# Optimization experiments

Hardware: AMD Instinct MI355X
Metric: run time of the kernel (lower is better)

The kernel has to match this reference:

```python
import jax, jax.numpy as jnp
import numpy as np

B = 131072      # batch size
H = 300         # hidden_dim (per-source), se has 2*H = 600 columns
T = 2           # num_source_tasks
EPS = 1e-20


def setup_inputs() -> dict:
    key = jax.random.key(0)
    k1, k2, k3, k4, k5 = jax.random.split(key, 5)
    return {
        "se1": jax.random.normal(k1, (B, H), dtype=jnp.float32),
        "se2": jax.random.normal(k2, (B, H), dtype=jnp.float32),
        "W": jax.random.normal(k3, (T, 2 * H), dtype=jnp.float32) / np.sqrt(2 * H).astype(np.float32),
        "b": jax.random.normal(k4, (T,), dtype=jnp.float32),
        "u": jax.random.uniform(k5, (B, T), dtype=jnp.float32),
        "n_tasks": 2,
    }


def reference(se1, se2, W, b, u, n_tasks):
    # se = torch.cat(se, dim=1) -> [B, 2H]
    se = jnp.concatenate([se1, se2], axis=1)
    # tiny linear + relu + log_softmax
    se_postrelu = jax.nn.relu(se @ W.T + b)            # [B, T]
    logits = jax.nn.log_softmax(se_postrelu, axis=1)   # [B, T]
    # straight-through gumbel-softmax (temperature=1.0, no mask)
    gumbel = -jnp.log(-jnp.log(u + EPS) + EPS)
    y = jax.nn.softmax(logits + gumbel, axis=1)        # soft probs
    y_hard = jax.nn.one_hot(jnp.argmax(y, axis=1), T, dtype=y.dtype)
    selector = jax.lax.stop_gradient(y_hard - y) + y   # ST estimator, [B, T]
    # rf: first H cols = selector[:,0], next H cols = selector[:,1]
    rf = jnp.repeat(selector, H, axis=1)               # [B, 2H]
    return se * rf
```

## Files before the change

### kernel.cpp

```cpp
#include <hip/hip_runtime.h>
#include <math.h>

#define BDIM 256
#define WPB (BDIM / 64)

__global__ __launch_bounds__(BDIM) void taskselector_kernel(
    const float* __restrict__ se1,
    const float* __restrict__ se2,
    const float* __restrict__ W,
    const float* __restrict__ bvec,
    const float* __restrict__ u,
    float* __restrict__ out,
    int Brows)
{
    const int lane   = threadIdx.x & 63;
    const int waveid = threadIdx.x >> 6;
    const int wglob  = blockIdx.x * WPB + waveid;
    const int nwaves = gridDim.x * WPB;

    const float4 zero4 = make_float4(0.f, 0.f, 0.f, 0.f);
    const bool extra = (lane < 11);

    const float4* W0 = reinterpret_cast<const float4*>(W);
    const float4* W1 = reinterpret_cast<const float4*>(W + 600);
    float4 w0a = W0[lane];
    float4 w0b = extra ? W0[64 + lane]  : zero4;
    float4 w0c = W0[75 + lane];
    float4 w0d = extra ? W0[139 + lane] : zero4;
    float4 w1a = W1[lane];
    float4 w1b = extra ? W1[64 + lane]  : zero4;
    float4 w1c = W1[75 + lane];
    float4 w1d = extra ? W1[139 + lane] : zero4;
    const float b0 = bvec[0];
    const float b1 = bvec[1];

    for (int row = wglob; row < Brows; row += nwaves) {
        const float4* p1 = reinterpret_cast<const float4*>(se1 + (size_t)row * 300);
        const float4* p2 = reinterpret_cast<const float4*>(se2 + (size_t)row * 300);

        float4 a0 = p1[lane];
        float4 a1 = extra ? p1[64 + lane] : zero4;
        float4 c0 = p2[lane];
        float4 c1 = extra ? p2[64 + lane] : zero4;

        float d0 = a0.x * w0a.x + a0.y * w0a.y + a0.z * w0a.z + a0.w * w0a.w
                 + a1.x * w0b.x + a1.y * w0b.y + a1.z * w0b.z + a1.w * w0b.w
                 + c0.x * w0c.x + c0.y * w0c.y + c0.z * w0c.z + c0.w * w0c.w
                 + c1.x * w0d.x + c1.y * w0d.y + c1.z * w0d.z + c1.w * w0d.w;
        float d1 = a0.x * w1a.x + a0.y * w1a.y + a0.z * w1a.z + a0.w * w1a.w
                 + a1.x * w1b.x + a1.y * w1b.y + a1.z * w1b.z + a1.w * w1b.w
                 + c0.x * w1c.x + c0.y * w1c.y + c0.z * w1c.z + c0.w * w1c.w
                 + c1.x * w1d.x + c1.y * w1d.y + c1.z * w1d.z + c1.w * w1d.w;

        #pragma unroll
        for (int off = 32; off > 0; off >>= 1) {
            d0 += __shfl_xor(d0, off, 64);
            d1 += __shfl_xor(d1, off, 64);
        }

        float z0 = fmaxf(d0 + b0, 0.f);
        float z1 = fmaxf(d1 + b1, 0.f);

        float m   = fmaxf(z0, z1);
        float lse = m + logf(expf(z0 - m) + expf(z1 - m));
        float l0  = z0 - lse;
        float l1  = z1 - lse;

        float u0 = u[(size_t)row * 2 + 0];
        float u1 = u[(size_t)row * 2 + 1];
        float g0 = -logf(-logf(u0 + 1e-20f) + 1e-20f);
        float g1 = -logf(-logf(u1 + 1e-20f) + 1e-20f);

        float q0 = l0 + g0;
        float q1 = l1 + g1;
        float mm = fmaxf(q0, q1);
        float e0 = expf(q0 - mm);
        float e1 = expf(q1 - mm);
        float s  = e0 + e1;
        float y0 = e0 / s;
        float y1 = e1 / s;

        bool  pick0 = (q0 >= q1);
        float s0 = pick0 ? ((1.f - y0) + y0) : 0.f;
        float s1 = pick0 ? 0.f : ((1.f - y1) + y1);

        float4* o = reinterpret_cast<float4*>(out + (size_t)row * 600);
        float4 r;
        r.x = a0.x * s0; r.y = a0.y * s0; r.z = a0.z * s0; r.w = a0.w * s0;
        o[lane] = r;
        if (extra) {
            r.x = a1.x * s0; r.y = a1.y * s0; r.z = a1.z * s0; r.w = a1.w * s0;
            o[64 + lane] = r;
        }
        r.x = c0.x * s1; r.y = c0.y * s1; r.z = c0.z * s1; r.w = c0.w * s1;
        o[75 + lane] = r;
        if (extra) {
            r.x = c1.x * s1; r.y = c1.y * s1; r.z = c1.z * s1; r.w = c1.w * s1;
            o[139 + lane] = r;
        }
    }
}

extern "C" void kernel_launch(void* const* d_in, const int* in_sizes, int n_in,
                              void* d_out, int out_size, void* d_ws, size_t ws_size,
                              hipStream_t stream) {
    const float* se1 = (const float*)d_in[0];
    const float* se2 = (const float*)d_in[1];
    const float* W   = (const float*)d_in[2];
    const float* b   = (const float*)d_in[3];
    const float* u   = (const float*)d_in[4];
    float* out = (float*)d_out;

    const int Brows = in_sizes[0] / 300;

    int blocks = 2048;
    int maxBlocks = (Brows + WPB - 1) / WPB;
    if (blocks > maxBlocks) blocks = maxBlocks;

    taskselector_kernel<<<blocks, BDIM, 0, stream>>>(se1, se2, W, b, u, out, Brows);
}
```

Baseline: 132.3 us.

## Process row pairs per wave with software-pipelined loads and nontemporal memory ops

Each wave now handles two rows at a time and works through a contiguous block of pairs instead of a strided set of rows. The next pair's loads are issued before the current pair is computed, giving a double-buffered software pipeline. Loads and stores use nontemporal hints, and the grid shrinks from 2048 to 512 blocks. The aim is more memory requests in flight per wave on a bandwidth-bound streaming kernel, at the cost of higher register pressure and fewer resident waves.

```diff
diff --git a/kernel.cpp b/kernel.cpp
--- a/kernel.cpp
+++ b/kernel.cpp
@@ -1,8 +1,103 @@
 #include <hip/hip_runtime.h>
 #include <math.h>
 
+typedef float f4 __attribute__((ext_vector_type(4)));
+
 #define BDIM 256
 #define WPB (BDIM / 64)
+#define NBLOCKS 512
+
+struct Pair {
+    f4 aA0, aA1, cA0, cA1, aB0, aB1, cB0, cB1, uu;
+};
+
+struct WReg {
+    f4 w0a, w0b, w0c, w0d, w1a, w1b, w1c, w1d;
+    float b0, b1;
+};
+
+__device__ __forceinline__ float dot4(f4 a, f4 w) {
+    return a[0]*w[0] + a[1]*w[1] + a[2]*w[2] + a[3]*w[3];
+}
+
+__device__ __forceinline__ void load_pair(Pair& P,
+        const float* __restrict__ se1, const float* __restrict__ se2,
+        const float* __restrict__ u, int pairIdx, int lane, bool extra)
+{
+    const int rowA = pairIdx * 2;
+    const f4* pA1 = (const f4*)(se1 + (size_t)rowA * 300);
+    const f4* pA2 = (const f4*)(se2 + (size_t)rowA * 300);
+    const f4* pB1 = pA1 + 75;
+    const f4* pB2 = pA2 + 75;
+    const f4 zero = (f4)0.f;
+    P.aA0 = __builtin_nontemporal_load(pA1 + lane);
+    P.cA0 = __builtin_nontemporal_load(pA2 + lane);
+    P.aB0 = __builtin_nontemporal_load(pB1 + lane);
+    P.cB0 = __builtin_nontemporal_load(pB2 + lane);
+    P.aA1 = zero; P.cA1 = zero; P.aB1 = zero; P.cB1 = zero;
+    if (extra) {
+        P.aA1 = __builtin_nontemporal_load(pA1 + 64 + lane);
+        P.cA1 = __builtin_nontemporal_load(pA2 + 64 + lane);
+        P.aB1 = __builtin_nontemporal_load(pB1 + 64 + lane);
+        P.cB1 = __builtin_nontemporal_load(pB2 + 64 + lane);
+    }
+    P.uu = *(const f4*)(u + (size_t)rowA * 2);
+}
+
+__device__ __forceinline__ void epilogue_row(float d0, float d1, float u0, float u1,
+                                             float b0, float b1, float& s0, float& s1)
+{
+    float z0 = fmaxf(d0 + b0, 0.f);
+    float z1 = fmaxf(d1 + b1, 0.f);
+    float m  = fmaxf(z0, z1);
+    float lse = m + logf(expf(z0 - m) + expf(z1 - m));
+    float q0 = (z0 - lse) + (-logf(-logf(u0 + 1e-20f) + 1e-20f));
+    float q1 = (z1 - lse) + (-logf(-logf(u1 + 1e-20f) + 1e-20f));
+    float mm = fmaxf(q0, q1);
+    float e0 = expf(q0 - mm);
+    float e1 = expf(q1 - mm);
+    float s  = e0 + e1;
+    float y0 = e0 / s;
+    float y1 = e1 / s;
+    bool  pick0 = (q0 >= q1);
+    s0 = pick0 ? ((1.f - y0) + y0) : 0.f;
+    s1 = pick0 ? 0.f : ((1.f - y1) + y1);
+}
+
+__device__ __forceinline__ void proc_pair(const Pair& P, const WReg& WR,
+        float* __restrict__ out, int pairIdx, int lane, bool extra)
+{
+    float dA0 = dot4(P.aA0, WR.w0a) + dot4(P.aA1, WR.w0b) + dot4(P.cA0, WR.w0c) + dot4(P.cA1, WR.w0d);
+    float dA1 = dot4(P.aA0, WR.w1a) + dot4(P.aA1, WR.w1b) + dot4(P.cA0, WR.w1c) + dot4(P.cA1, WR.w1d);
+    float dB0 = dot4(P.aB0, WR.w0a) + dot4(P.aB1, WR.w0b) + dot4(P.cB0, WR.w0c) + dot4(P.cB1, WR.w0d);
+    float dB1 = dot4(P.aB0, WR.w1a) + dot4(P.aB1, WR.w1b) + dot4(P.cB0, WR.w1c) + dot4(P.cB1, WR.w1d);
+
+    #pragma unroll
+    for (int off = 32; off > 0; off >>= 1) {
+        dA0 += __shfl_xor(dA0, off, 64);
+        dA1 += __shfl_xor(dA1, off, 64);
+        dB0 += __shfl_xor(dB0, off, 64);
+        dB1 += __shfl_xor(dB1, off, 64);
+    }
+
+    float sA0, sA1, sB0, sB1;
+    epilogue_row(dA0, dA1, P.uu[0], P.uu[1], WR.b0, WR.b1, sA0, sA1);
+    epilogue_row(dB0, dB1, P.uu[2], P.uu[3], WR.b0, WR.b1, sB0, sB1);
+
+    const int rowA = pairIdx * 2;
+    f4* oA = (f4*)(out + (size_t)rowA * 600);
+    f4* oB = oA + 150;
+    __builtin_nontemporal_store(P.aA0 * sA0, oA + lane);
+    __builtin_nontemporal_store(P.cA0 * sA1, oA + 75 + lane);
+    __builtin_nontemporal_store(P.aB0 * sB0, oB + lane);
+    __builtin_nontemporal_store(P.cB0 * sB1, oB + 75 + lane);
+    if (extra) {
+        __builtin_nontemporal_store(P.aA1 * sA0, oA + 64 + lane);
+        __builtin_nontemporal_store(P.cA1 * sA1, oA + 139 + lane);
+        __builtin_nontemporal_store(P.aB1 * sB0, oB + 64 + lane);
+        __builtin_nontemporal_store(P.cB1 * sB1, oB + 139 + lane);
+    }
+}
 
 __global__ __launch_bounds__(BDIM) void taskselector_kernel(
     const float* __restrict__ se1,
@@ -16,87 +111,73 @@
     const int lane   = threadIdx.x & 63;
     const int waveid = threadIdx.x >> 6;
     const int wglob  = blockIdx.x * WPB + waveid;
-    const int nwaves = gridDim.x * WPB;
-
-    const float4 zero4 = make_float4(0.f, 0.f, 0.f, 0.f);
+    const int nw     = gridDim.x * WPB;
     const bool extra = (lane < 11);
-
-    const float4* W0 = reinterpret_cast<const float4*>(W);
-    const float4* W1 = reinterpret_cast<const float4*>(W + 600);
-    float4 w0a = W0[lane];
-    float4 w0b = extra ? W0[64 + lane]  : zero4;
-    float4 w0c = W0[75 + lane];
-    float4 w0d = extra ? W0[139 + lane] : zero4;
-    float4 w1a = W1[lane];
-    float4 w1b = extra ? W1[64 + lane]  : zero4;
-    float4 w1c = W1[75 + lane];
-    float4 w1d = extra ? W1[139 + lane] : zero4;
-    const float b0 = bvec[0];
-    const float b1 = bvec[1];
-
-    for (int row = wglob; row < Brows; row += nwaves) {
-        const float4* p1 = reinterpret_cast<const float4*>(se1 + (size_t)row * 300);
-        const float4* p2 = reinterpret_cast<const float4*>(se2 + (size_t)row * 300);
-
-        float4 a0 = p1[lane];
-        float4 a1 = extra ? p1[64 + lane] : zero4;
-        float4 c0 = p2[lane];
-        float4 c1 = extra ? p2[64 + lane] : zero4;
-
-        float d0 = a0.x * w0a.x + a0.y * w0a.y + a0.z * w0a.z + a0.w * w0a.w
-                 + a1.x * w0b.x + a1.y * w0b.y + a1.z * w0b.z + a1.w * w0b.w
-                 + c0.x * w0c.x + c0.y * w0c.y + c0.z * w0c.z + c0.w * w0c.w
-                 + c1.x * w0d.x + c1.y * w0d.y + c1.z * w0d.z + c1.w * w0d.w;
-        float d1 = a0.x * w1a.x + a0.y * w1a.y + a0.z * w1a.z + a0.w * w1a.w
-                 + a1.x * w1b.x + a1.y * w1b.y + a1.z * w1b.z + a1.w * w1b.w
-                 + c0.x * w1c.x + c0.y * w1c.y + c0.z * w1c.z + c0.w * w1c.w
-                 + c1.x * w1d.x + c1.y * w1d.y + c1.z * w1d.z + c1.w * w1d.w;
-
+    const f4 zero = (f4)0.f;
+
+    WReg WR;
+    const f4* W0 = (const f4*)(W);
+    const f4* W1 = (const f4*)(W + 600);
+    WR.w0a = W0[lane];
+    WR.w0b = extra ? W0[64 + lane]  : zero;
+    WR.w0c = W0[75 + lane];
+    WR.w0d = extra ? W0[139 + lane] : zero;
+    WR.w1a = W1[lane];
+    WR.w1b = extra ? W1[64 + lane]  : zero;
+    WR.w1c = W1[75 + lane];
+    WR.w1d = extra ? W1[139 + lane] : zero;
+    WR.b0 = bvec[0];
+    WR.b1 = bvec[1];
+
+    const int pairsTotal = Brows >> 1;
+    const int ppw = pairsTotal / nw;
+    const int rem = pairsTotal - ppw * nw;
+    int i   = wglob * ppw + (wglob < rem ? wglob : rem);
+    int cnt = ppw + (wglob < rem ? 1 : 0);
+
+    if (cnt > 0) {
+        const int end = i + cnt;
+        Pair X, Y;
+        load_pair(X, se1, se2, u, i, lane, extra);
+        while (i + 2 < end) {
+            load_pair(Y, se1, se2, u, i + 1, lane, extra);
+            proc_pair(X, WR, out, i, lane, extra);
+            load_pair(X, se1, se2, u, i + 2, lane, extra);
+            proc_pair(Y, WR, out, i + 1, lane, extra);
+            i += 2;
+        }
+        if (end - i == 2) {
+            load_pair(Y, se1, se2, u, i + 1, lane, extra);
+            proc_pair(X, WR, out, i, lane, extra);
+            proc_pair(Y, WR, out, i + 1, lane, extra);
+        } else {
+            proc_pair(X, WR, out, i, lane, extra);
+        }
+    }
+
+    if ((Brows & 1) && wglob == 0) {
+        const int row = Brows - 1;
+        const f4* p1 = (const f4*)(se1 + (size_t)row * 300);
+        const f4* p2 = (const f4*)(se2 + (size_t)row * 300);
+        f4 a0 = p1[lane];
+        f4 c0 = p2[lane];
+        f4 a1 = extra ? p1[64 + lane] : zero;
+        f4 c1 = extra ? p2[64 + lane] : zero;
+        float d0 = dot4(a0, WR.w0a) + dot4(a1, WR.w0b) + dot4(c0, WR.w0c) + dot4(c1, WR.w0d);
+        float d1 = dot4(a0, WR.w1a) + dot4(a1, WR.w1b) + dot4(c0, WR.w1c) + dot4(c1, WR.w1d);
         #pragma unroll
         for (int off = 32; off > 0; off >>= 1) {
             d0 += __shfl_xor(d0, off, 64);
             d1 += __shfl_xor(d1, off, 64);
         }
-
-        float z0 = fmaxf(d0 + b0, 0.f);
-        float z1 = fmaxf(d1 + b1, 0.f);
-
-        float m   = fmaxf(z0, z1);
-        float lse = m + logf(expf(z0 - m) + expf(z1 - m));
-        float l0  = z0 - lse;
-        float l1  = z1 - lse;
-
-        float u0 = u[(size_t)row * 2 + 0];
-        float u1 = u[(size_t)row * 2 + 1];
-        float g0 = -logf(-logf(u0 + 1e-20f) + 1e-20f);
-        float g1 = -logf(-logf(u1 + 1e-20f) + 1e-20f);
-
-        float q0 = l0 + g0;
-        float q1 = l1 + g1;
-        float mm = fmaxf(q0, q1);
-        float e0 = expf(q0 - mm);
-        float e1 = expf(q1 - mm);
-        float s  = e0 + e1;
-        float y0 = e0 / s;
-        float y1 = e1 / s;
-
-        bool  pick0 = (q0 >= q1);
-        float s0 = pick0 ? ((1.f - y0) + y0) : 0.f;
-        float s1 = pick0 ? 0.f : ((1.f - y1) + y1);
-
-        float4* o = reinterpret_cast<float4*>(out + (size_t)row * 600);
-        float4 r;
-        r.x = a0.x * s0; r.y = a0.y * s0; r.z = a0.z * s0; r.w = a0.w * s0;
-        o[lane] = r;
+        float s0, s1;
+        epilogue_row(d0, d1, u[(size_t)row * 2], u[(size_t)row * 2 + 1], WR.b0, WR.b1, s0, s1);
+        f4* o = (f4*)(out + (size_t)row * 600);
+        o[lane] = a0 * s0;
+        o[75 + lane] = c0 * s1;
         if (extra) {
-            r.x = a1.x * s0; r.y = a1.y * s0; r.z = a1.z * s0; r.w = a1.w * s0;
-            o[64 + lane] = r;
-        }
-        r.x = c0.x * s1; r.y = c0.y * s1; r.z = c0.z * s1; r.w = c0.w * s1;
-        o[75 + lane] = r;
-        if (extra) {
-            r.x = c1.x * s1; r.y = c1.y * s1; r.z = c1.z * s1; r.w = c1.w * s1;
-            o[139 + lane] = r;
+            o[64 + lane]  = a1 * s0;
+            o[139 + lane] = c1 * s1;
         }
     }
 }
@@ -113,8 +194,8 @@
 
     const int Brows = in_sizes[0] / 300;
 
-    int blocks = 2048;
-    int maxBlocks = (Brows + WPB - 1) / WPB;
+    int blocks = NBLOCKS;
+    int maxBlocks = ((Brows >> 1) + WPB - 1) / WPB;
     if (blocks > maxBlocks) blocks = maxBlocks;
 
     taskselector_kernel<<<blocks, BDIM, 0, stream>>>(se1, se2, W, b, u, out, Brows);
```

After: 142.5 us. +7.7%, slower.

## Stage 16-row tiles in LDS with coalesced nontemporal loads and stores

Applied to the files above, without the earlier changes.

Each block now takes a 16-row tile and loads it with fully coalesced nontemporal float4 loads into shared memory. Dot products and the selector are computed from LDS, and the output is written back as one contiguous coalesced nontemporal stream, with one block per tile instead of a grid-stride loop over rows. This removes partially idle lanes and scattered 1200-byte row accesses, and bypasses cache for streaming data. In exchange it uses about 38KB of LDS per block, which limits occupancy, adds two barriers, and assumes the batch size is divisible by 16.

```diff
diff --git a/kernel.cpp b/kernel.cpp
--- a/kernel.cpp
+++ b/kernel.cpp
@@ -1,121 +1,146 @@
 #include <hip/hip_runtime.h>
 #include <math.h>
 
+typedef float f4 __attribute__((ext_vector_type(4)));
+
 #define BDIM 256
-#define WPB (BDIM / 64)
+#define TROWS 16
+#define RPW 4
+#define TILE_F4_IN 1200
+#define TILE_F4_OUT 2400
+
+__device__ __forceinline__ float dot4(f4 a, f4 w) {
+    return a[0]*w[0] + a[1]*w[1] + a[2]*w[2] + a[3]*w[3];
+}
 
 __global__ __launch_bounds__(BDIM) void taskselector_kernel(
-    const float* __restrict__ se1,
-    const float* __restrict__ se2,
+    const f4* __restrict__ se1,
+    const f4* __restrict__ se2,
     const float* __restrict__ W,
     const float* __restrict__ bvec,
-    const float* __restrict__ u,
-    float* __restrict__ out,
-    int Brows)
+    const f4* __restrict__ u4,
+    f4* __restrict__ out)
 {
-    const int lane   = threadIdx.x & 63;
-    const int waveid = threadIdx.x >> 6;
-    const int wglob  = blockIdx.x * WPB + waveid;
-    const int nwaves = gridDim.x * WPB;
+    __shared__ f4 L1[TILE_F4_IN];
+    __shared__ f4 L2[TILE_F4_IN];
+    __shared__ float SEL[TROWS * 2];
+    __shared__ f4 UL[TROWS / 2];
 
-    const float4 zero4 = make_float4(0.f, 0.f, 0.f, 0.f);
+    const int tid  = threadIdx.x;
+    const int lane = tid & 63;
+    const int wave = tid >> 6;
+    const int tile = blockIdx.x;
+
     const bool extra = (lane < 11);
-
-    const float4* W0 = reinterpret_cast<const float4*>(W);
-    const float4* W1 = reinterpret_cast<const float4*>(W + 600);
-    float4 w0a = W0[lane];
-    float4 w0b = extra ? W0[64 + lane]  : zero4;
-    float4 w0c = W0[75 + lane];
-    float4 w0d = extra ? W0[139 + lane] : zero4;
-    float4 w1a = W1[lane];
-    float4 w1b = extra ? W1[64 + lane]  : zero4;
-    float4 w1c = W1[75 + lane];
-    float4 w1d = extra ? W1[139 + lane] : zero4;
+    const f4 zero = (f4)0.f;
+    const f4* W0 = (const f4*)W;
+    const f4* W1 = (const f4*)(W + 600);
+    f4 w0a = W0[lane];
+    f4 w0b = extra ? W0[64 + lane]  : zero;
+    f4 w0c = W0[75 + lane];
+    f4 w0d = extra ? W0[139 + lane] : zero;
+    f4 w1a = W1[lane];
+    f4 w1b = extra ? W1[64 + lane]  : zero;
+    f4 w1c = W1[75 + lane];
+    f4 w1d = extra ? W1[139 + lane] : zero;
     const float b0 = bvec[0];
     const float b1 = bvec[1];
 
-    for (int row = wglob; row < Brows; row += nwaves) {
-        const float4* p1 = reinterpret_cast<const float4*>(se1 + (size_t)row * 300);
-        const float4* p2 = reinterpret_cast<const float4*>(se2 + (size_t)row * 300);
+    const f4* s1 = se1 + (size_t)tile * TILE_F4_IN;
+    const f4* s2 = se2 + (size_t)tile * TILE_F4_IN;
+    f4 t[4], q[4];
+    #pragma unroll
+    for (int k = 0; k < 4; k++) t[k] = __builtin_nontemporal_load(s1 + k * BDIM + tid);
+    #pragma unroll
+    for (int k = 0; k < 4; k++) q[k] = __builtin_nontemporal_load(s2 + k * BDIM + tid);
+    f4 t4 = zero, q4 = zero;
+    if (tid < TILE_F4_IN - 4 * BDIM) {
+        t4 = __builtin_nontemporal_load(s1 + 4 * BDIM + tid);
+        q4 = __builtin_nontemporal_load(s2 + 4 * BDIM + tid);
+    }
+    if (tid < TROWS / 2) UL[tid] = u4[(size_t)tile * (TROWS / 2) + tid];
+    #pragma unroll
+    for (int k = 0; k < 4; k++) L1[k * BDIM + tid] = t[k];
+    #pragma unroll
+    for (int k = 0; k < 4; k++) L2[k * BDIM + tid] = q[k];
+    if (tid < TILE_F4_IN - 4 * BDIM) {
+        L1[4 * BDIM + tid] = t4;
+        L2[4 * BDIM + tid] = q4;
+    }
+    __syncthreads();
 
-        float4 a0 = p1[lane];
-        float4 a1 = extra ? p1[64 + lane] : zero4;
-        float4 c0 = p2[lane];
-        float4 c1 = extra ? p2[64 + lane] : zero4;
-
-        float d0 = a0.x * w0a.x + a0.y * w0a.y + a0.z * w0a.z + a0.w * w0a.w
-                 + a1.x * w0b.x + a1.y * w0b.y + a1.z * w0b.z + a1.w * w0b.w
-                 + c0.x * w0c.x + c0.y * w0c.y + c0.z * w0c.z + c0.w * w0c.w
-                 + c1.x * w0d.x + c1.y * w0d.y + c1.z * w0d.z + c1.w * w0d.w;
-        float d1 = a0.x * w1a.x + a0.y * w1a.y + a0.z * w1a.z + a0.w * w1a.w
-                 + a1.x * w1b.x + a1.y * w1b.y + a1.z * w1b.z + a1.w * w1b.w
-                 + c0.x * w1c.x + c0.y * w1c.y + c0.z * w1c.z + c0.w * w1c.w
-                 + c1.x * w1d.x + c1.y * w1d.y + c1.z * w1d.z + c1.w * w1d.w;
-
+    const float* ULf = (const float*)UL;
+    #pragma unroll
+    for (int rr = 0; rr < RPW; rr++) {
+        const int r = wave * RPW + rr;
+        const f4* R1 = L1 + r * 75;
+        const f4* R2 = L2 + r * 75;
+        f4 a0 = R1[lane];
+        f4 c0 = R2[lane];
+        f4 a1 = extra ? R1[64 + lane] : zero;
+        f4 c1 = extra ? R2[64 + lane] : zero;
+        float d0 = dot4(a0, w0a) + dot4(a1, w0b) + dot4(c0, w0c) + dot4(c1, w0d);
+        float d1 = dot4(a0, w1a) + dot4(a1, w1b) + dot4(c0, w1c) + dot4(c1, w1d);
         #pragma unroll
         for (int off = 32; off > 0; off >>= 1) {
             d0 += __shfl_xor(d0, off, 64);
             d1 += __shfl_xor(d1, off, 64);
         }
-
         float z0 = fmaxf(d0 + b0, 0.f);
         float z1 = fmaxf(d1 + b1, 0.f);
-
-        float m   = fmaxf(z0, z1);
+        float m  = fmaxf(z0, z1);
         float lse = m + logf(expf(z0 - m) + expf(z1 - m));
-        float l0  = z0 - lse;
-        float l1  = z1 - lse;
-
-        float u0 = u[(size_t)row * 2 + 0];
-        float u1 = u[(size_t)row * 2 + 1];
-        float g0 = -logf(-logf(u0 + 1e-20f) + 1e-20f);
-        float g1 = -logf(-logf(u1 + 1e-20f) + 1e-20f);
-
-        float q0 = l0 + g0;
-        float q1 = l1 + g1;
+        float uu0 = ULf[2 * r];
+        float uu1 = ULf[2 * r + 1];
+        float q0 = (z0 - lse) + (-logf(-logf(uu0 + 1e-20f) + 1e-20f));
+        float q1 = (z1 - lse) + (-logf(-logf(uu1 + 1e-20f) + 1e-20f));
         float mm = fmaxf(q0, q1);
         float e0 = expf(q0 - mm);
         float e1 = expf(q1 - mm);
         float s  = e0 + e1;
         float y0 = e0 / s;
         float y1 = e1 / s;
-
         bool  pick0 = (q0 >= q1);
         float s0 = pick0 ? ((1.f - y0) + y0) : 0.f;
-        float s1 = pick0 ? 0.f : ((1.f - y1) + y1);
+        float s1v = pick0 ? 0.f : ((1.f - y1) + y1);
+        if (lane == 0) { SEL[2 * r] = s0; SEL[2 * r + 1] = s1v; }
+    }
+    __syncthreads();
 
-        float4* o = reinterpret_cast<float4*>(out + (size_t)row * 600);
-        float4 r;
-        r.x = a0.x * s0; r.y = a0.y * s0; r.z = a0.z * s0; r.w = a0.w * s0;
-        o[lane] = r;
-        if (extra) {
-            r.x = a1.x * s0; r.y = a1.y * s0; r.z = a1.z * s0; r.w = a1.w * s0;
-            o[64 + lane] = r;
-        }
-        r.x = c0.x * s1; r.y = c0.y * s1; r.z = c0.z * s1; r.w = c0.w * s1;
-        o[75 + lane] = r;
-        if (extra) {
-            r.x = c1.x * s1; r.y = c1.y * s1; r.z = c1.z * s1; r.w = c1.w * s1;
-            o[139 + lane] = r;
-        }
+    f4* o = out + (size_t)tile * TILE_F4_OUT;
+    #pragma unroll
+    for (int k = 0; k < 9; k++) {
+        const int j   = k * BDIM + tid;
+        const int row = j / 150;
+        const int rem = j - row * 150;
+        const bool first = (rem < 75);
+        f4 v = first ? L1[row * 75 + rem] : L2[row * 75 + rem - 75];
+        float sc = SEL[2 * row + (first ? 0 : 1)];
+        __builtin_nontemporal_store(v * sc, o + j);
+    }
+    if (tid < TILE_F4_OUT - 9 * BDIM) {
+        const int j   = 9 * BDIM + tid;
+        const int row = j / 150;
+        const int rem = j - row * 150;
+        const bool first = (rem < 75);
+        f4 v = first ? L1[row * 75 + rem] : L2[row * 75 + rem - 75];
+        float sc = SEL[2 * row + (first ? 0 : 1)];
+        __builtin_nontemporal_store(v * sc, o + j);
     }
 }
 
 extern "C" void kernel_launch(void* const* d_in, const int* in_sizes, int n_in,
                               void* d_out, int out_size, void* d_ws, size_t ws_size,
                               hipStream_t stream) {
-    const float* se1 = (const float*)d_in[0];
-    const float* se2 = (const float*)d_in[1];
-    const float* W   = (const float*)d_in[2];
-    const float* b   = (const float*)d_in[3];
-    const float* u   = (const float*)d_in[4];
-    float* out = (float*)d_out;
+    const f4* se1 = (const f4*)d_in[0];
+    const f4* se2 = (const f4*)d_in[1];
+    const float* W = (const float*)d_in[2];
+    const float* b = (const float*)d_in[3];
+    const f4* u4  = (const f4*)d_in[4];
+    f4* out = (f4*)d_out;
 
     const int Brows = in_sizes[0] / 300;
+    const int ntiles = Brows / TROWS;
 
-    int blocks = 2048;
-    int maxBlocks = (Brows + WPB - 1) / WPB;
-    if (blocks > maxBlocks) blocks = maxBlocks;
-
-    taskselector_kernel<<<blocks, BDIM, 0, stream>>>(se1, se2, W, b, u, out, Brows);
+    taskselector_kernel<<<ntiles, BDIM, 0, stream>>>(se1, se2, W, b, u4, out);
 }
```

New measurement: 111.3 us. -15.9%, faster.
